# Kernel optimization log

Measured on AMD Instinct MI355X. Metric: run time of the kernel, lower is better.

Reference implementation:

```python
import jax, jax.numpy as jnp
import numpy as np

B, S, D, H = 2, 2048, 1024, 16
DH = D // H
LN_EPS = 1e-12


def setup_inputs() -> dict:
    key = jax.random.key(0)
    ks = jax.random.split(key, 12)
    sc = 1.0 / np.sqrt(D)
    return {
        "hidden_states": jax.random.normal(ks[0], (B, S, D), jnp.float32),
        "attention_mask": jnp.zeros((B, 1, 1, S), jnp.float32),
        "Wq": jax.random.normal(ks[1], (D, D), jnp.float32) * sc,
        "bq": jnp.zeros((D,), jnp.float32),
        "Wk": jax.random.normal(ks[2], (D, D), jnp.float32) * sc,
        "bk": jnp.zeros((D,), jnp.float32),
        "Wv": jax.random.normal(ks[3], (D, D), jnp.float32) * sc,
        "bv": jnp.zeros((D,), jnp.float32),
        "Wo": jax.random.normal(ks[4], (D, D), jnp.float32) * sc,
        "bo": jnp.zeros((D,), jnp.float32),
        "ln_w": jnp.ones((D,), jnp.float32),
        "ln_b": jnp.zeros((D,), jnp.float32),
    }


def _split_heads(x):
    # [B,S,D] -> [B,H,S,DH]
    return x.reshape(B, S, H, DH).transpose(0, 2, 1, 3)


def reference(hidden_states, attention_mask, Wq, bq, Wk, bk, Wv, bv, Wo, bo, ln_w, ln_b):
    q = _split_heads(hidden_states @ Wq + bq)
    k = _split_heads(hidden_states @ Wk + bk)
    v = _split_heads(hidden_states @ Wv + bv)
    scores = jnp.einsum("bhqd,bhkd->bhqk", q, k) / np.sqrt(DH)
    scores = scores + attention_mask
    probs = jax.nn.softmax(scores, axis=-1)  # dropout prob=0 -> identity
    ctx = jnp.einsum("bhqk,bhkd->bhqd", probs, v)
    ctx = ctx.transpose(0, 2, 1, 3).reshape(B, S, D)
    # output dense + residual + LayerNorm (biased variance, per original)
    h = ctx @ Wo + bo + hidden_states
    u = h.mean(-1, keepdims=True)
    s = ((h - u) ** 2).mean(-1, keepdims=True)
    out = ln_w * ((h - u) / jnp.sqrt(s + LN_EPS)) + ln_b
    return out, probs
```

## Files before the change

kernel.cpp:

```cpp
#include <hip/hip_runtime.h>
#include <stdint.h>


typedef __attribute__((ext_vector_type(8))) short short8;
typedef __attribute__((ext_vector_type(4))) float f32x4;

__device__ __forceinline__ unsigned short f2b(float f) {
  union { float f; unsigned u; } v; v.f = f;
  unsigned u = v.u;
  return (unsigned short)((u + 0x7fffu + ((u >> 16) & 1u)) >> 16);
}

__global__ void k_cast_hs(const float* __restrict__ x, unsigned short* __restrict__ y, int n4) {
  int i = blockIdx.x * blockDim.x + threadIdx.x;
  if (i < n4) {
    float4 v = ((const float4*)x)[i];
    ushort4 o;
    o.x = f2b(v.x); o.y = f2b(v.y); o.z = f2b(v.z); o.w = f2b(v.w);
    ((ushort4*)y)[i] = o;
  }
}

__global__ void k_transpose_cast(const float* __restrict__ Wq, const float* __restrict__ Wk,
                                 const float* __restrict__ Wv, const float* __restrict__ Wo,
                                 unsigned short* __restrict__ Tq, unsigned short* __restrict__ Tk,
                                 unsigned short* __restrict__ Tv, unsigned short* __restrict__ To) {
  __shared__ float tile[32][33];
  const float* W; unsigned short* T;
  switch (blockIdx.z) {
    case 0: W = Wq; T = Tq; break;
    case 1: W = Wk; T = Tk; break;
    case 2: W = Wv; T = Tv; break;
    default: W = Wo; T = To; break;
  }
  int n0 = blockIdx.x * 32, k0 = blockIdx.y * 32;
  int tx = threadIdx.x, ty = threadIdx.y;
#pragma unroll
  for (int j = 0; j < 4; ++j)
    tile[ty + j * 8][tx] = W[(size_t)(k0 + ty + j * 8) * 1024 + n0 + tx];
  __syncthreads();
#pragma unroll
  for (int j = 0; j < 4; ++j)
    T[(size_t)(n0 + ty + j * 8) * 1024 + k0 + tx] = f2b(tile[tx][ty + j * 8]);
}

template <int MODE>
__global__ __launch_bounds__(256) void k_gemm(const unsigned short* __restrict__ A,
                                              const unsigned short* __restrict__ Bt, int Kd,
                                              const float* __restrict__ bias,
                                              const float* __restrict__ resid,
                                              void* __restrict__ outp, float qscale) {
  __shared__ __align__(16) unsigned short Asm[128 * 32];
  __shared__ __align__(16) unsigned short Bsm[128 * 32];
  const int t = threadIdx.x, w = t >> 6, l = t & 63;
  const int m0 = blockIdx.y * 128, n0 = blockIdx.x * 128;
  const int wr = w >> 1, wc = w & 1;
  const int lr = l & 15, lg = l >> 4;

  f32x4 acc[4][4];
#pragma unroll
  for (int mi = 0; mi < 4; ++mi)
#pragma unroll
    for (int ni = 0; ni < 4; ++ni) acc[mi][ni] = (f32x4){0.f, 0.f, 0.f, 0.f};

  const int kcol = (l & 3) * 8;
  for (int kt = 0; kt < Kd / 32; ++kt) {
    const int k0 = kt * 32;
#pragma unroll
    for (int i = 0; i < 2; ++i) {
      int ra = (i * 4 + w) * 16 + (l >> 2);
      const unsigned short* ga = A + (size_t)(m0 + ra) * Kd + k0 + kcol;
      __builtin_amdgcn_global_load_lds((const __attribute__((address_space(1))) void*)ga,
                                       (__attribute__((address_space(3))) void*)((char*)Asm + (i * 4 + w) * 1024),
                                       16, 0, 0);
      const unsigned short* gb = Bt + (size_t)(n0 + ra) * Kd + k0 + kcol;
      __builtin_amdgcn_global_load_lds((const __attribute__((address_space(1))) void*)gb,
                                       (__attribute__((address_space(3))) void*)((char*)Bsm + (i * 4 + w) * 1024),
                                       16, 0, 0);
    }
    __syncthreads();
    short8 af[4], bfv[4];
#pragma unroll
    for (int mi = 0; mi < 4; ++mi)
      af[mi] = *(const short8*)&Asm[(wr * 64 + mi * 16 + lr) * 32 + lg * 8];
#pragma unroll
    for (int ni = 0; ni < 4; ++ni)
      bfv[ni] = *(const short8*)&Bsm[(wc * 64 + ni * 16 + lr) * 32 + lg * 8];
#pragma unroll
    for (int mi = 0; mi < 4; ++mi)
#pragma unroll
      for (int ni = 0; ni < 4; ++ni)
        acc[mi][ni] = __builtin_amdgcn_mfma_f32_16x16x32_bf16(af[mi], bfv[ni], acc[mi][ni], 0, 0, 0);
    __syncthreads();
  }

#pragma unroll
  for (int mi = 0; mi < 4; ++mi) {
#pragma unroll
    for (int ni = 0; ni < 4; ++ni) {
#pragma unroll
      for (int r = 0; r < 4; ++r) {
        int row = m0 + wr * 64 + mi * 16 + lg * 4 + r;
        int col = n0 + wc * 64 + ni * 16 + lr;
        float v = acc[mi][ni][r];
        if constexpr (MODE == 0) {
          v = (v + bias[col]) * qscale;
          int b = row >> 11, s = row & 2047, h = col >> 6, dh = col & 63;
          ((unsigned short*)outp)[((size_t)((b * 16 + h) * 2048 + s)) * 64 + dh] = f2b(v);
        } else if constexpr (MODE == 1) {
          v += bias[row];
          int h = row >> 6, dh = row & 63, b = col >> 11, s = col & 2047;
          ((unsigned short*)outp)[((size_t)((b * 16 + h) * 64 + dh)) * 2048 + s] = f2b(v);
        } else {
          v += bias[col] + resid[(size_t)row * 1024 + col];
          ((float*)outp)[(size_t)row * 1024 + col] = v;
        }
      }
    }
  }
}

__global__ __launch_bounds__(256, 2) void k_attn(const unsigned short* __restrict__ Q,
                                                 const unsigned short* __restrict__ K,
                                                 const unsigned short* __restrict__ VT,
                                                 const float* __restrict__ mask,
                                                 float* __restrict__ probs,
                                                 unsigned short* __restrict__ ctx) {
  __shared__ float smax[4][16];
  __shared__ float ssum[4][16];
  __shared__ __align__(16) char shbuf[33792];
  unsigned short (*pbuf)[16][264] = (unsigned short(*)[16][264])shbuf;
  float (*redbuf)[16][64] = (float(*)[16][64])shbuf;

  const int t = threadIdx.x, w = t >> 6, l = t & 63;
  const int qb = blockIdx.x, h = blockIdx.y, b = blockIdx.z;
  const int q0 = qb * 16;
  const int lr = l & 15, lg = l >> 4;
  const size_t head = ((size_t)(b * 16 + h)) * 2048 * 64;
  const unsigned short* Qh = Q + head + (size_t)q0 * 64;
  const unsigned short* Kh = K + head;
  const unsigned short* VTh = VT + head;

  short8 aq0 = *(const short8*)(Qh + lr * 64 + lg * 8);
  short8 aq1 = *(const short8*)(Qh + lr * 64 + 32 + lg * 8);

  f32x4 sc[32];
#pragma unroll
  for (int ni = 0; ni < 32; ++ni) {
    int col = w * 512 + ni * 16 + lr;
    short8 bk0 = *(const short8*)(Kh + (size_t)col * 64 + lg * 8);
    short8 bk1 = *(const short8*)(Kh + (size_t)col * 64 + 32 + lg * 8);
    f32x4 c = (f32x4){0.f, 0.f, 0.f, 0.f};
    c = __builtin_amdgcn_mfma_f32_16x16x32_bf16(bk0, aq0, c, 0, 0, 0);
    c = __builtin_amdgcn_mfma_f32_16x16x32_bf16(bk1, aq1, c, 0, 0, 0);
    f32x4 mv = *(const f32x4*)(mask + b * 2048 + w * 512 + ni * 16 + lg * 4);
    sc[ni] = c + mv;
  }

  float vmax = -1e30f;
#pragma unroll
  for (int ni = 0; ni < 32; ++ni)
#pragma unroll
    for (int r = 0; r < 4; ++r) vmax = fmaxf(vmax, sc[ni][r]);
  vmax = fmaxf(vmax, __shfl_xor(vmax, 16));
  vmax = fmaxf(vmax, __shfl_xor(vmax, 32));
  if (l < 16) smax[w][l] = vmax;
  __syncthreads();
  float m = fmaxf(fmaxf(smax[0][lr], smax[1][lr]), fmaxf(smax[2][lr], smax[3][lr]));

  float vsum = 0.f;
#pragma unroll
  for (int ni = 0; ni < 32; ++ni)
#pragma unroll
    for (int r = 0; r < 4; ++r) {
      float p = __expf(sc[ni][r] - m);
      sc[ni][r] = p;
      vsum += p;
    }
  vsum += __shfl_xor(vsum, 16);
  vsum += __shfl_xor(vsum, 32);
  if (l < 16) ssum[w][l] = vsum;
  __syncthreads();
  float rinv = 1.f / (ssum[0][lr] + ssum[1][lr] + ssum[2][lr] + ssum[3][lr]);

#pragma unroll
  for (int ni = 0; ni < 32; ++ni) sc[ni] *= rinv;

  {
    float* prow = probs + ((size_t)((b * 16 + h) * 2048 + q0 + lr)) * 2048 + w * 512 + lg * 4;
#pragma unroll
    for (int ni = 0; ni < 32; ++ni)
      *(f32x4*)(prow + ni * 16) = sc[ni];
  }

  f32x4 cacc[4];
#pragma unroll
  for (int n = 0; n < 4; ++n) cacc[n] = (f32x4){0.f, 0.f, 0.f, 0.f};

#pragma unroll
  for (int chunk = 0; chunk < 2; ++chunk) {
#pragma unroll
    for (int ni2 = 0; ni2 < 16; ++ni2) {
      int ni = chunk * 16 + ni2;
      ushort4 pk;
      pk.x = f2b(sc[ni][0]); pk.y = f2b(sc[ni][1]);
      pk.z = f2b(sc[ni][2]); pk.w = f2b(sc[ni][3]);
      *(ushort4*)&pbuf[w][lr][ni2 * 16 + lg * 4] = pk;
    }
#pragma unroll
    for (int kc = 0; kc < 8; ++kc) {
      short8 pa = *(const short8*)&pbuf[w][lr][kc * 32 + lg * 8];
      size_t kg = (size_t)w * 512 + chunk * 256 + kc * 32;
#pragma unroll
      for (int n = 0; n < 4; ++n) {
        short8 bv = *(const short8*)(VTh + (size_t)(n * 16 + lr) * 2048 + kg + lg * 8);
        cacc[n] = __builtin_amdgcn_mfma_f32_16x16x32_bf16(pa, bv, cacc[n], 0, 0, 0);
      }
    }
  }
  __syncthreads();

#pragma unroll
  for (int n = 0; n < 4; ++n)
#pragma unroll
    for (int r = 0; r < 4; ++r)
      redbuf[w][lg * 4 + r][n * 16 + lr] = cacc[n][r];
  __syncthreads();

  {
    int row = t >> 4;
    int c0 = (t & 15) * 4;
    float v0 = redbuf[0][row][c0] + redbuf[1][row][c0] + redbuf[2][row][c0] + redbuf[3][row][c0];
    float v1 = redbuf[0][row][c0 + 1] + redbuf[1][row][c0 + 1] + redbuf[2][row][c0 + 1] + redbuf[3][row][c0 + 1];
    float v2 = redbuf[0][row][c0 + 2] + redbuf[1][row][c0 + 2] + redbuf[2][row][c0 + 2] + redbuf[3][row][c0 + 2];
    float v3 = redbuf[0][row][c0 + 3] + redbuf[1][row][c0 + 3] + redbuf[2][row][c0 + 3] + redbuf[3][row][c0 + 3];
    ushort4 o;
    o.x = f2b(v0); o.y = f2b(v1); o.z = f2b(v2); o.w = f2b(v3);
    *(ushort4*)(ctx + ((size_t)(b * 2048 + q0 + row)) * 1024 + h * 64 + c0) = o;
  }
}

__global__ __launch_bounds__(256) void k_ln(const float* __restrict__ hbuf, const float* __restrict__ g,
                                            const float* __restrict__ be, float* __restrict__ out) {
  __shared__ float psum[4];
  __shared__ float psq[4];
  int tok = blockIdx.x;
  int t = threadIdx.x, w = t >> 6;
  float4 v = ((const float4*)(hbuf + (size_t)tok * 1024))[t];
  float s = v.x + v.y + v.z + v.w;
  float q = v.x * v.x + v.y * v.y + v.z * v.z + v.w * v.w;
#pragma unroll
  for (int off = 32; off >= 1; off >>= 1) {
    s += __shfl_xor(s, off);
    q += __shfl_xor(q, off);
  }
  if ((t & 63) == 0) { psum[w] = s; psq[w] = q; }
  __syncthreads();
  float S = psum[0] + psum[1] + psum[2] + psum[3];
  float Qs = psq[0] + psq[1] + psq[2] + psq[3];
  float u = S * (1.f / 1024.f);
  float var = Qs * (1.f / 1024.f) - u * u;
  float rstd = rsqrtf(var + 1e-12f);
  float4 gv = ((const float4*)g)[t];
  float4 bv = ((const float4*)be)[t];
  float4 o;
  o.x = gv.x * ((v.x - u) * rstd) + bv.x;
  o.y = gv.y * ((v.y - u) * rstd) + bv.y;
  o.z = gv.z * ((v.z - u) * rstd) + bv.z;
  o.w = gv.w * ((v.w - u) * rstd) + bv.w;
  ((float4*)(out + (size_t)tok * 1024))[t] = o;
}

extern "C" void kernel_launch(void* const* d_in, const int* in_sizes, int n_in,
                              void* d_out, int out_size, void* d_ws, size_t ws_size,
                              hipStream_t stream) {
  const float* hs   = (const float*)d_in[0];
  const float* mask = (const float*)d_in[1];
  const float* Wq   = (const float*)d_in[2];
  const float* bq   = (const float*)d_in[3];
  const float* Wk   = (const float*)d_in[4];
  const float* bk   = (const float*)d_in[5];
  const float* Wv   = (const float*)d_in[6];
  const float* bv   = (const float*)d_in[7];
  const float* Wo   = (const float*)d_in[8];
  const float* bo   = (const float*)d_in[9];
  const float* lnw  = (const float*)d_in[10];
  const float* lnb  = (const float*)d_in[11];

  float* out = (float*)d_out;
  float* probs = out + (size_t)4194304;

  char* ws = (char*)d_ws;
  const size_t MB = 1u << 20;
  unsigned short* hsb = (unsigned short*)(ws + 0 * MB);
  unsigned short* TqW = (unsigned short*)(ws + 8 * MB);
  unsigned short* TkW = (unsigned short*)(ws + 10 * MB);
  unsigned short* TvW = (unsigned short*)(ws + 12 * MB);
  unsigned short* ToW = (unsigned short*)(ws + 14 * MB);
  unsigned short* Qb  = (unsigned short*)(ws + 16 * MB);
  unsigned short* Kb  = (unsigned short*)(ws + 24 * MB);
  unsigned short* VTb = (unsigned short*)(ws + 32 * MB);
  unsigned short* ctxb = (unsigned short*)(ws + 40 * MB);
  float* hbuf = (float*)(ws + 48 * MB);

  k_cast_hs<<<4096, 256, 0, stream>>>(hs, hsb, 1048576);
  k_transpose_cast<<<dim3(32, 32, 4), dim3(32, 8), 0, stream>>>(Wq, Wk, Wv, Wo, TqW, TkW, TvW, ToW);

  k_gemm<0><<<dim3(8, 32), 256, 0, stream>>>(hsb, TqW, 1024, bq, nullptr, Qb, 0.125f);
  k_gemm<0><<<dim3(8, 32), 256, 0, stream>>>(hsb, TkW, 1024, bk, nullptr, Kb, 1.0f);
  k_gemm<1><<<dim3(32, 8), 256, 0, stream>>>(TvW, hsb, 1024, bv, nullptr, VTb, 1.0f);

  k_attn<<<dim3(128, 16, 2), 256, 0, stream>>>(Qb, Kb, VTb, mask, probs, ctxb);

  k_gemm<2><<<dim3(8, 32), 256, 0, stream>>>(ctxb, ToW, 1024, bo, hs, hbuf, 1.0f);
  k_ln<<<4096, 256, 0, stream>>>(hbuf, lnw, lnb, out);
}
```

Before: 559.6 us.

## Stage bf16 probs in shared memory and write coalesced nontemporal fp32 rows

```diff
diff --git a/kernel.cpp b/kernel.cpp
--- a/kernel.cpp
+++ b/kernel.cpp
@@ -9,6 +9,12 @@
   union { float f; unsigned u; } v; v.f = f;
   unsigned u = v.u;
   return (unsigned short)((u + 0x7fffu + ((u >> 16) & 1u)) >> 16);
+}
+
+__device__ __forceinline__ float b2f(unsigned short s) {
+  union { unsigned u; float f; } v;
+  v.u = ((unsigned)s) << 16;
+  return v.f;
 }
 
 __global__ void k_cast_hs(const float* __restrict__ x, unsigned short* __restrict__ y, int n4) {
@@ -128,9 +134,8 @@
                                                  unsigned short* __restrict__ ctx) {
   __shared__ float smax[4][16];
   __shared__ float ssum[4][16];
-  __shared__ __align__(16) char shbuf[33792];
-  unsigned short (*pbuf)[16][264] = (unsigned short(*)[16][264])shbuf;
-  float (*redbuf)[16][64] = (float(*)[16][64])shbuf;
+  __shared__ __align__(16) unsigned short Pall[16][2056];
+  float (*redbuf)[16][64] = (float(*)[16][64])Pall;
 
   const int t = threadIdx.x, w = t >> 6, l = t & 63;
   const int qb = blockIdx.x, h = blockIdx.y, b = blockIdx.z;
@@ -184,37 +189,47 @@
   float rinv = 1.f / (ssum[0][lr] + ssum[1][lr] + ssum[2][lr] + ssum[3][lr]);
 
 #pragma unroll
-  for (int ni = 0; ni < 32; ++ni) sc[ni] *= rinv;
+  for (int ni = 0; ni < 32; ++ni) {
+    float p0 = sc[ni][0] * rinv, p1 = sc[ni][1] * rinv;
+    float p2 = sc[ni][2] * rinv, p3 = sc[ni][3] * rinv;
+    ushort4 pk;
+    pk.x = f2b(p0); pk.y = f2b(p1); pk.z = f2b(p2); pk.w = f2b(p3);
+    *(ushort4*)&Pall[lr][w * 512 + ni * 16 + lg * 4] = pk;
+  }
+  __syncthreads();
+
+  f32x4 cacc[4];
+#pragma unroll
+  for (int n = 0; n < 4; ++n) cacc[n] = (f32x4){0.f, 0.f, 0.f, 0.f};
+
+#pragma unroll
+  for (int kc = 0; kc < 16; ++kc) {
+    short8 pa = *(const short8*)&Pall[lr][w * 512 + kc * 32 + lg * 8];
+    size_t kg = (size_t)w * 512 + kc * 32;
+#pragma unroll
+    for (int n = 0; n < 4; ++n) {
+      short8 bv = *(const short8*)(VTh + (size_t)(n * 16 + lr) * 2048 + kg + lg * 8);
+      cacc[n] = __builtin_amdgcn_mfma_f32_16x16x32_bf16(pa, bv, cacc[n], 0, 0, 0);
+    }
+  }
 
   {
-    float* prow = probs + ((size_t)((b * 16 + h) * 2048 + q0 + lr)) * 2048 + w * 512 + lg * 4;
-#pragma unroll
-    for (int ni = 0; ni < 32; ++ni)
-      *(f32x4*)(prow + ni * 16) = sc[ni];
-  }
-
-  f32x4 cacc[4];
-#pragma unroll
-  for (int n = 0; n < 4; ++n) cacc[n] = (f32x4){0.f, 0.f, 0.f, 0.f};
-
-#pragma unroll
-  for (int chunk = 0; chunk < 2; ++chunk) {
-#pragma unroll
-    for (int ni2 = 0; ni2 < 16; ++ni2) {
-      int ni = chunk * 16 + ni2;
-      ushort4 pk;
-      pk.x = f2b(sc[ni][0]); pk.y = f2b(sc[ni][1]);
-      pk.z = f2b(sc[ni][2]); pk.w = f2b(sc[ni][3]);
-      *(ushort4*)&pbuf[w][lr][ni2 * 16 + lg * 4] = pk;
-    }
-#pragma unroll
-    for (int kc = 0; kc < 8; ++kc) {
-      short8 pa = *(const short8*)&pbuf[w][lr][kc * 32 + lg * 8];
-      size_t kg = (size_t)w * 512 + chunk * 256 + kc * 32;
-#pragma unroll
-      for (int n = 0; n < 4; ++n) {
-        short8 bv = *(const short8*)(VTh + (size_t)(n * 16 + lr) * 2048 + kg + lg * 8);
-        cacc[n] = __builtin_amdgcn_mfma_f32_16x16x32_bf16(pa, bv, cacc[n], 0, 0, 0);
+    const size_t prow0 = ((size_t)((b * 16 + h) * 2048 + q0)) * 2048;
+#pragma unroll
+    for (int rr = 0; rr < 4; ++rr) {
+      int row = w * 4 + rr;
+      float* gp = probs + prow0 + (size_t)row * 2048;
+#pragma unroll
+      for (int p = 0; p < 4; ++p) {
+        short8 pv = *(const short8*)&Pall[row][p * 512 + l * 8];
+        f32x4 o0, o1;
+        o0[0] = b2f((unsigned short)pv[0]); o0[1] = b2f((unsigned short)pv[1]);
+        o0[2] = b2f((unsigned short)pv[2]); o0[3] = b2f((unsigned short)pv[3]);
+        o1[0] = b2f((unsigned short)pv[4]); o1[1] = b2f((unsigned short)pv[5]);
+        o1[2] = b2f((unsigned short)pv[6]); o1[3] = b2f((unsigned short)pv[7]);
+        f32x4* dst = (f32x4*)(gp + p * 512 + l * 8);
+        __builtin_nontemporal_store(o0, dst);
+        __builtin_nontemporal_store(o1, dst + 1);
       }
     }
   }
```

New measurement: 456.0 us. 1.23x faster.
